# Performance work log

Measured on AMD Instinct MI355X. Metric: run time of the kernel, lower is better.

The kernel has to match this reference:

```python
import jax, jax.numpy as jnp
import numpy as np
import math

B, S, D, H = 8, 1024, 1024, 16
DH = D // H  # 64


def setup_inputs() -> dict:
    key = jax.random.key(0)
    ks = jax.random.split(key, 10)
    inputs = jax.random.normal(ks[0], (B, S, D), dtype=jnp.float32)
    mask = jax.random.randint(ks[1], (B, S, S), 0, 2) == 1  # bool [B,S,S]
    sc = 1.0 / math.sqrt(D)
    # per-head projection weights stacked: [H, D, DH], biases [H, DH]
    Wq = jax.random.normal(ks[2], (H, D, DH), dtype=jnp.float32) * sc
    bq = jax.random.normal(ks[3], (H, DH), dtype=jnp.float32) * 0.02
    Wk = jax.random.normal(ks[4], (H, D, DH), dtype=jnp.float32) * sc
    bk = jax.random.normal(ks[5], (H, DH), dtype=jnp.float32) * 0.02
    Wv = jax.random.normal(ks[6], (H, D, DH), dtype=jnp.float32) * sc
    bv = jax.random.normal(ks[7], (H, DH), dtype=jnp.float32) * 0.02
    Wo = jax.random.normal(ks[8], (D, D), dtype=jnp.float32) * sc
    bo = jax.random.normal(ks[9], (D,), dtype=jnp.float32) * 0.02
    return {"inputs": inputs, "mask": mask, "Wq": Wq, "bq": bq, "Wk": Wk,
            "bk": bk, "Wv": Wv, "bv": bv, "Wo": Wo, "bo": bo}


def reference(inputs, mask, Wq, bq, Wk, bk, Wv, bv, Wo, bo):
    d_model = inputs.shape[-1]
    scale = 1.0 / jnp.sqrt(jnp.asarray(d_model, inputs.dtype))  # note: sqrt(d_model), as in source
    # batched per-head projections: [B,H,S,DH]
    Q = jnp.einsum('bsd,hde->bhse', inputs, Wq) + bq[None, :, None, :]
    K = jnp.einsum('bsd,hde->bhse', inputs, Wk) + bk[None, :, None, :]
    V = jnp.einsum('bsd,hde->bhse', inputs, Wv) + bv[None, :, None, :]
    scores = jnp.einsum('bhse,bhte->bhst', Q, K) * scale  # [B,H,S,S]
    scores = jnp.where(mask[:, None, :, :], jnp.asarray(-1e9, scores.dtype), scores)
    attn = jax.nn.softmax(scores, axis=-1)
    ctx = jnp.einsum('bhst,bhte->bhse', attn, V)  # [B,H,S,DH]
    # concat heads along last dim (head h -> slice h*DH:(h+1)*DH), matches torch.cat
    bsz, h, s, dh = ctx.shape
    x = ctx.transpose(0, 2, 1, 3).reshape(bsz, s, h * dh)
    return x @ Wo + bo
```

## Files before the change

kernel.cpp:

```cpp
#include <hip/hip_runtime.h>
#include <hip/hip_bf16.h>
#include <stdint.h>


typedef __attribute__((ext_vector_type(8))) short short8;
typedef __attribute__((ext_vector_type(4))) float floatx4;

__device__ __forceinline__ int swz(int r, int kc) { return r * 8 + (kc ^ (r & 7)); }
__device__ __forceinline__ short8 as_frag(uint4 u) { return __builtin_bit_cast(short8, u); }
__device__ __forceinline__ floatx4 mfma16(short8 a, short8 b, floatx4 c) {
    return __builtin_amdgcn_mfma_f32_16x16x32_bf16(a, b, c, 0, 0, 0);
}
__device__ __forceinline__ unsigned short f2bu(float f) {
    return __builtin_bit_cast(unsigned short, __float2bfloat16(f));
}
__device__ __forceinline__ short f2b(float f) {
    return __builtin_bit_cast(short, __float2bfloat16(f));
}
__device__ __forceinline__ float b2f(short s) {
    return __bfloat162float(__builtin_bit_cast(__hip_bfloat16, s));
}
__device__ __forceinline__ void dma16(const void* g, void* l) {
    __builtin_amdgcn_global_load_lds(
        (const __attribute__((address_space(1))) uint32_t*)g,
        (__attribute__((address_space(3))) uint32_t*)l, 16, 0, 0);
}
__device__ __forceinline__ uint2 pack4(float a, float b, float c, float d) {
    uint2 p;
    p.x = (unsigned)f2bu(a) | ((unsigned)f2bu(b) << 16);
    p.y = (unsigned)f2bu(c) | ((unsigned)f2bu(d) << 16);
    return p;
}

__device__ __forceinline__ void detect_mode(const unsigned* Xw, int* s_is32) {
    if (threadIdx.x < 64) {
        unsigned lo = Xw[threadIdx.x] & 0xFFFFu;
        unsigned e = (lo >> 7) & 0xFFu;
        unsigned long long bal = __ballot(e >= 88u && e <= 150u);
        if (threadIdx.x == 0) *s_is32 = (bal != ~0ull) ? 1 : 0;
    }
    __syncthreads();
}

__device__ __forceinline__ float load_elt(const void* p, size_t idx, int is32) {
    return is32 ? ((const float*)p)[idx]
                : __bfloat162float(((const __hip_bfloat16*)p)[idx]);
}

__global__ __launch_bounds__(256) void transpose_weights(
    const void* __restrict__ Wq, const void* __restrict__ Wk,
    const void* __restrict__ Wv, const void* __restrict__ Wo,
    const unsigned* __restrict__ Xw,
    __hip_bfloat16* __restrict__ WT, __hip_bfloat16* __restrict__ WoT)
{
    __shared__ int s_is32;
    detect_mode(Xw, &s_is32);
    __shared__ __hip_bfloat16 T[64][72];
    int blk = blockIdx.x;
    const void* src; size_t src_off;
    __hip_bfloat16* dst;
    int src_ld, dst_ld;
    if (blk < 768) {
        int p = blk >> 8;
        int rem = blk & 255;
        int h = rem >> 4, dt = rem & 15;
        src = (p == 0) ? Wq : (p == 1) ? Wk : Wv;
        src_off = ((size_t)h * 1024 + (size_t)dt * 64) * 64;
        dst = WT + (((size_t)p * 16 + h) * 64) * 1024 + dt * 64;
        src_ld = 64; dst_ld = 1024;
    } else {
        int t = blk - 768;
        int kt = t >> 4, nt = t & 15;
        src = Wo; src_off = (size_t)kt * 64 * 1024 + nt * 64;
        dst = WoT + (size_t)nt * 64 * 1024 + kt * 64;
        src_ld = 1024; dst_ld = 1024;
    }
    int tid = threadIdx.x;
    #pragma unroll
    for (int i = 0; i < 16; i++) {
        int idx = tid + i * 256;
        int r = idx >> 6, c = idx & 63;
        T[c][r] = __float2bfloat16(load_elt(src, src_off + (size_t)r * src_ld + c, s_is32));
    }
    __syncthreads();
    #pragma unroll
    for (int i = 0; i < 16; i++) {
        int idx = tid + i * 256;
        int r = idx >> 6, c = idx & 63;
        dst[(size_t)r * dst_ld + c] = T[r][c];
    }
}

__global__ __launch_bounds__(256) void convert_bias(
    const void* __restrict__ bq, const void* __restrict__ bk,
    const void* __restrict__ bv, const void* __restrict__ bo,
    const unsigned* __restrict__ Xw, __hip_bfloat16* __restrict__ bc)
{
    __shared__ int s_is32;
    detect_mode(Xw, &s_is32);
    int tid = threadIdx.x;
    #pragma unroll
    for (int i = 0; i < 16; i++) {
        int idx = tid + i * 256;
        int which = idx >> 10, j = idx & 1023;
        const void* src = (which == 0) ? bq : (which == 1) ? bk : (which == 2) ? bv : bo;
        bc[idx] = __float2bfloat16(load_elt(src, j, s_is32));
    }
}

__global__ __launch_bounds__(256) void prep_mask(
    const void* __restrict__ mask_raw, unsigned long long* __restrict__ bits64)
{
    const int* mi = (const int*)mask_raw;
    const unsigned char* mb = (const unsigned char*)mask_raw;
    int tid = threadIdx.x, lane = tid & 63;
    bool ok = true;
    #pragma unroll
    for (int i = 0; i < 4; i++) {
        unsigned v = (unsigned)mi[lane * 4 + i];
        if (v > 1u) ok = false;
    }
    bool is_i32 = (__ballot(ok) == ~0ull);
    int gw = (blockIdx.x * 256 + tid) >> 6;
    const int NW = 512 * 4;
    const int NWORDS = (8 * 1024 * 1024) / 64;
    if (is_i32) {
        for (int i = gw; i < NWORDS; i += NW) {
            int mv = mi[(size_t)i * 64 + lane];
            unsigned long long bal = __ballot(mv != 0);
            if (lane == 0) bits64[i] = bal;
        }
    } else {
        for (int i = gw; i < NWORDS; i += NW) {
            int mv = mb[(size_t)i * 64 + lane];
            unsigned long long bal = __ballot(mv != 0);
            if (lane == 0) bits64[i] = bal;
        }
    }
}

__global__ __launch_bounds__(256) void convert_x(
    const void* __restrict__ X, __hip_bfloat16* __restrict__ Xb)
{
    __shared__ int s_is32;
    detect_mode((const unsigned*)X, &s_is32);
    size_t g = ((size_t)blockIdx.x * 256 + threadIdx.x) * 16;
    if (s_is32) {
        const float* Xf = (const float*)X;
        #pragma unroll
        for (int half = 0; half < 2; half++) {
            float4 f0 = *(const float4*)(Xf + g + half * 8);
            float4 f1 = *(const float4*)(Xf + g + half * 8 + 4);
            short8 s;
            s[0] = f2b(f0.x); s[1] = f2b(f0.y); s[2] = f2b(f0.z); s[3] = f2b(f0.w);
            s[4] = f2b(f1.x); s[5] = f2b(f1.y); s[6] = f2b(f1.z); s[7] = f2b(f1.w);
            *(uint4*)(Xb + g + half * 8) = __builtin_bit_cast(uint4, s);
        }
    } else {
        const uint4* Xu = (const uint4*)X;
        *(uint4*)(Xb + g)     = Xu[g / 8];
        *(uint4*)(Xb + g + 8) = Xu[g / 8 + 1];
    }
}

__global__ __launch_bounds__(256) void qkv_gemm_dma(
    const __hip_bfloat16* __restrict__ Xb,
    const __hip_bfloat16* __restrict__ WT,
    const __hip_bfloat16* __restrict__ bc,
    __hip_bfloat16* __restrict__ Q,
    __hip_bfloat16* __restrict__ Ko,
    __hip_bfloat16* __restrict__ Vt)
{
    __shared__ uint4 AsU[128 * 8];
    __shared__ uint4 BsU[128 * 8];
    int tid = threadIdx.x, lane = tid & 63, wave = tid >> 6;
    int quad = lane >> 4, ln = lane & 15;
    int m0 = blockIdx.x * 128;
    int n0 = blockIdx.y * 128;
    const __hip_bfloat16* Wp = WT + (size_t)n0 * 1024;

    floatx4 acc[2][8];
    #pragma unroll
    for (int i = 0; i < 2; i++)
        #pragma unroll
        for (int j = 0; j < 8; j++) acc[i][j] = (floatx4){0.f, 0.f, 0.f, 0.f};

    for (int k0 = 0; k0 < 1024; k0 += 64) {
        #pragma unroll
        for (int i = 0; i < 4; i++) {
            int r = wave * 32 + i * 8 + (lane >> 3);
            int kc = (lane & 7) ^ (r & 7);
            char* ldsA = (char*)AsU + (size_t)(wave * 256 + i * 64) * 16;
            char* ldsB = (char*)BsU + (size_t)(wave * 256 + i * 64) * 16;
            dma16(Xb + (size_t)(m0 + r) * 1024 + k0 + kc * 8, ldsA);
            dma16(Wp + (size_t)r * 1024 + k0 + kc * 8, ldsB);
        }
        __syncthreads();
        #pragma unroll
        for (int kk = 0; kk < 2; kk++) {
            short8 a0 = as_frag(AsU[swz(wave * 32 + ln, kk * 4 + quad)]);
            short8 a1 = as_frag(AsU[swz(wave * 32 + 16 + ln, kk * 4 + quad)]);
            #pragma unroll
            for (int nt = 0; nt < 8; nt++) {
                short8 bf = as_frag(BsU[swz(nt * 16 + ln, kk * 4 + quad)]);
                acc[0][nt] = mfma16(a0, bf, acc[0][nt]);
                acc[1][nt] = mfma16(a1, bf, acc[1][nt]);
            }
        }
        __syncthreads();
    }

    int b = m0 >> 10;
    int s0 = m0 & 1023;
    int proj = n0 >> 10;
    if (proj == 2) {
        #pragma unroll
        for (int nt = 0; nt < 8; nt++) {
            int n = n0 + nt * 16 + ln;
            int h = (n >> 6) & 15, e = n & 63;
            float bval = __bfloat162float(bc[2 * 1024 + (n & 1023)]);
            #pragma unroll
            for (int mt = 0; mt < 2; mt++) {
                int sb = s0 + wave * 32 + mt * 16 + quad * 4;
                uint2 pk = pack4(acc[mt][nt][0] + bval, acc[mt][nt][1] + bval,
                                 acc[mt][nt][2] + bval, acc[mt][nt][3] + bval);
                *(uint2*)(Vt + (((size_t)b * 16 + h) * 64 + e) * 1024 + sb) = pk;
            }
        }
    } else {
        __hip_bfloat16* P = (proj == 0) ? Q : Ko;
        #pragma unroll
        for (int nt = 0; nt < 8; nt++) {
            int n = n0 + nt * 16 + ln;
            int h = (n >> 6) & 15, e = n & 63;
            float bval = __bfloat162float(bc[proj * 1024 + (n & 1023)]);
            #pragma unroll
            for (int mt = 0; mt < 2; mt++) {
                #pragma unroll
                for (int r = 0; r < 4; r++) {
                    int s = s0 + wave * 32 + mt * 16 + quad * 4 + r;
                    P[(((size_t)b * 16 + h) * 1024 + s) * 64 + e] =
                        __float2bfloat16(acc[mt][nt][r] + bval);
                }
            }
        }
    }
}

__global__ __launch_bounds__(256) void qkv_gemm2(
    const void* __restrict__ Xsrc,
    const __hip_bfloat16* __restrict__ WT,
    const __hip_bfloat16* __restrict__ bc,
    __hip_bfloat16* __restrict__ Q,
    __hip_bfloat16* __restrict__ Ko,
    __hip_bfloat16* __restrict__ Vt)
{
    __shared__ int s_is32;
    detect_mode((const unsigned*)Xsrc, &s_is32);
    __shared__ uint4 AsU[128 * 8];
    __shared__ uint4 BsU[128 * 8];
    int tid = threadIdx.x, lane = tid & 63, wave = tid >> 6;
    int quad = lane >> 4, ln = lane & 15;
    int m0 = blockIdx.x * 128;
    int n0 = blockIdx.y * 128;
    const __hip_bfloat16* Wp = WT + (size_t)n0 * 1024;
    const float* Xf = (const float*)Xsrc;
    const __hip_bfloat16* Xh = (const __hip_bfloat16*)Xsrc;

    floatx4 acc[2][8];
    #pragma unroll
    for (int i = 0; i < 2; i++)
        #pragma unroll
        for (int j = 0; j < 8; j++) acc[i][j] = (floatx4){0.f, 0.f, 0.f, 0.f};

    for (int k0 = 0; k0 < 1024; k0 += 64) {
        if (s_is32) {
            #pragma unroll
            for (int i = 0; i < 4; i++) {
                int id = tid + i * 256;
                int r = id >> 3, kc = id & 7;
                size_t off = (size_t)(m0 + r) * 1024 + k0 + kc * 8;
                float4 f0 = *(const float4*)(Xf + off);
                float4 f1 = *(const float4*)(Xf + off + 4);
                short8 s;
                s[0] = f2b(f0.x); s[1] = f2b(f0.y); s[2] = f2b(f0.z); s[3] = f2b(f0.w);
                s[4] = f2b(f1.x); s[5] = f2b(f1.y); s[6] = f2b(f1.z); s[7] = f2b(f1.w);
                AsU[swz(r, kc)] = __builtin_bit_cast(uint4, s);
            }
        } else {
            #pragma unroll
            for (int i = 0; i < 4; i++) {
                int id = tid + i * 256;
                int r = id >> 3, kc = id & 7;
                AsU[swz(r, kc)] = *(const uint4*)(Xh + (size_t)(m0 + r) * 1024 + k0 + kc * 8);
            }
        }
        #pragma unroll
        for (int i = 0; i < 4; i++) {
            int id = tid + i * 256;
            int r = id >> 3, kc = id & 7;
            BsU[swz(r, kc)] = *(const uint4*)(Wp + (size_t)r * 1024 + k0 + kc * 8);
        }
        __syncthreads();
        #pragma unroll
        for (int kk = 0; kk < 2; kk++) {
            short8 a0 = as_frag(AsU[swz(wave * 32 + ln, kk * 4 + quad)]);
            short8 a1 = as_frag(AsU[swz(wave * 32 + 16 + ln, kk * 4 + quad)]);
            #pragma unroll
            for (int nt = 0; nt < 8; nt++) {
                short8 bf = as_frag(BsU[swz(nt * 16 + ln, kk * 4 + quad)]);
                acc[0][nt] = mfma16(a0, bf, acc[0][nt]);
                acc[1][nt] = mfma16(a1, bf, acc[1][nt]);
            }
        }
        __syncthreads();
    }

    int b = m0 >> 10;
    int s0 = m0 & 1023;
    #pragma unroll
    for (int nt = 0; nt < 8; nt++) {
        int n = n0 + nt * 16 + ln;
        int proj = n >> 10, h = (n >> 6) & 15, e = n & 63;
        float bval = __bfloat162float(bc[proj * 1024 + (n & 1023)]);
        #pragma unroll
        for (int mt = 0; mt < 2; mt++) {
            #pragma unroll
            for (int r = 0; r < 4; r++) {
                int s = s0 + wave * 32 + mt * 16 + quad * 4 + r;
                float v = acc[mt][nt][r] + bval;
                if (proj == 2) {
                    Vt[(((size_t)b * 16 + h) * 64 + e) * 1024 + s] = __float2bfloat16(v);
                } else {
                    __hip_bfloat16* P = (proj == 0) ? Q : Ko;
                    P[(((size_t)b * 16 + h) * 1024 + s) * 64 + e] = __float2bfloat16(v);
                }
            }
        }
    }
}

__global__ __launch_bounds__(256) void attn(
    const __hip_bfloat16* __restrict__ Q,
    const __hip_bfloat16* __restrict__ K,
    const __hip_bfloat16* __restrict__ Vt,
    const unsigned long long* __restrict__ bits,
    __hip_bfloat16* __restrict__ ctx)
{
    __shared__ uint4 QsU[128 * 8];
    __shared__ uint4 KsU[64 * 8];
    __shared__ uint4 VsU[64 * 8];
    __shared__ __hip_bfloat16 Ps[4 * 32 * 72];
    __shared__ unsigned long long Ms[128];

    int tid = threadIdx.x, lane = tid & 63, wave = tid >> 6;
    int quad = lane >> 4, ln = lane & 15;
    int bh = blockIdx.x;
    int q0 = blockIdx.y * 128;
    int b = bh >> 4, h = bh & 15;
    const __hip_bfloat16* Qp = Q + (size_t)bh * 1024 * 64;
    const __hip_bfloat16* Kp = K + (size_t)bh * 1024 * 64;
    const __hip_bfloat16* Vp = Vt + (size_t)bh * 64 * 1024;
    const unsigned long long* bp = bits + (size_t)b * 1024 * 16;

    #pragma unroll
    for (int i = 0; i < 4; i++) {
        int r = wave * 32 + i * 8 + (lane >> 3);
        int kc = (lane & 7) ^ (r & 7);
        char* lds = (char*)QsU + (size_t)(wave * 256 + i * 64) * 16;
        dma16(Qp + (size_t)(q0 + r) * 64 + kc * 8, lds);
    }
    __syncthreads();
    short8 qf[2][2];
    #pragma unroll
    for (int g = 0; g < 2; g++)
        #pragma unroll
        for (int kk = 0; kk < 2; kk++)
            qf[g][kk] = as_frag(QsU[swz(wave * 32 + g * 16 + ln, kk * 4 + quad)]);

    floatx4 acc_o[2][4];
    #pragma unroll
    for (int g = 0; g < 2; g++)
        #pragma unroll
        for (int i = 0; i < 4; i++) acc_o[g][i] = (floatx4){0.f, 0.f, 0.f, 0.f};
    float lsum[2] = {0.f, 0.f};
    const float scale = 0.03125f;
    __hip_bfloat16* Pw = Ps + wave * (32 * 72);

    for (int t0 = 0; t0 < 1024; t0 += 64) {
        __syncthreads();
        #pragma unroll
        for (int i = 0; i < 2; i++) {
            int r = (wave * 2 + i) * 8 + (lane >> 3);
            int kc = (lane & 7) ^ (r & 7);
            char* ldsK = (char*)KsU + (size_t)((wave * 2 + i) * 64) * 16;
            char* ldsV = (char*)VsU + (size_t)((wave * 2 + i) * 64) * 16;
            dma16(Kp + (size_t)(t0 + r) * 64 + kc * 8, ldsK);
            dma16(Vp + (size_t)r * 1024 + t0 + kc * 8, ldsV);
        }
        if (tid < 128)
            Ms[tid] = bp[(size_t)(q0 + tid) * 16 + (t0 >> 6)];
        __syncthreads();

        floatx4 st[2][4];
        #pragma unroll
        for (int g = 0; g < 2; g++)
            #pragma unroll
            for (int i = 0; i < 4; i++) st[g][i] = (floatx4){0.f, 0.f, 0.f, 0.f};
        #pragma unroll
        for (int kk = 0; kk < 2; kk++) {
            #pragma unroll
            for (int tt = 0; tt < 4; tt++) {
                short8 kf = as_frag(KsU[swz(tt * 16 + ln, kk * 4 + quad)]);
                st[0][tt] = mfma16(kf, qf[0][kk], st[0][tt]);
                st[1][tt] = mfma16(kf, qf[1][kk], st[1][tt]);
            }
        }

        #pragma unroll
        for (int g = 0; g < 2; g++) {
            unsigned long long mw = Ms[wave * 32 + g * 16 + ln];
            #pragma unroll
            for (int tt = 0; tt < 4; tt++) {
                unsigned mb = (unsigned)(mw >> (tt * 16 + quad * 4)) & 0xFu;
                float pe0 = (mb & 1u) ? 0.f : __expf(st[g][tt][0] * scale);
                float pe1 = (mb & 2u) ? 0.f : __expf(st[g][tt][1] * scale);
                float pe2 = (mb & 4u) ? 0.f : __expf(st[g][tt][2] * scale);
                float pe3 = (mb & 8u) ? 0.f : __expf(st[g][tt][3] * scale);
                lsum[g] += (pe0 + pe1) + (pe2 + pe3);
                *(uint2*)(Pw + (g * 16 + ln) * 72 + tt * 16 + quad * 4) =
                    pack4(pe0, pe1, pe2, pe3);
            }
        }

        #pragma unroll
        for (int kk = 0; kk < 2; kk++) {
            short8 pf0 = as_frag(*(const uint4*)(Pw + (0 * 16 + ln) * 72 + kk * 32 + quad * 8));
            short8 pf1 = as_frag(*(const uint4*)(Pw + (1 * 16 + ln) * 72 + kk * 32 + quad * 8));
            #pragma unroll
            for (int et = 0; et < 4; et++) {
                short8 vf = as_frag(VsU[swz(et * 16 + ln, kk * 4 + quad)]);
                acc_o[0][et] = mfma16(vf, pf0, acc_o[0][et]);
                acc_o[1][et] = mfma16(vf, pf1, acc_o[1][et]);
            }
        }
    }

    #pragma unroll
    for (int g = 0; g < 2; g++) {
        lsum[g] += __shfl_xor(lsum[g], 16, 64);
        lsum[g] += __shfl_xor(lsum[g], 32, 64);
    }
    float inv[2];
    inv[0] = 1.f / fmaxf(lsum[0], 1e-20f);
    inv[1] = 1.f / fmaxf(lsum[1], 1e-20f);

    #pragma unroll
    for (int g = 0; g < 2; g++) {
        int s = q0 + wave * 32 + g * 16 + ln;
        __hip_bfloat16* crow = ctx + ((size_t)b * 1024 + s) * 1024 + h * 64 + quad * 4;
        #pragma unroll
        for (int et = 0; et < 4; et++) {
            uint2 pk = pack4(acc_o[g][et][0] * inv[g], acc_o[g][et][1] * inv[g],
                             acc_o[g][et][2] * inv[g], acc_o[g][et][3] * inv[g]);
            *(uint2*)(crow + et * 16) = pk;
        }
    }
}

__global__ __launch_bounds__(256) void out_gemm_dma(
    const __hip_bfloat16* __restrict__ Cx,
    const __hip_bfloat16* __restrict__ WoT,
    const __hip_bfloat16* __restrict__ bc,
    const unsigned* __restrict__ Xw,
    void* __restrict__ dout,
    int direct)
{
    __shared__ int s_is32;
    detect_mode(Xw, &s_is32);
    __shared__ uint4 AsU[128 * 8];
    __shared__ uint4 BsU[128 * 8];
    int tid = threadIdx.x, lane = tid & 63, wave = tid >> 6;
    int quad = lane >> 4, ln = lane & 15;
    int m0 = blockIdx.x * 128;
    int n0 = blockIdx.y * 128;

    floatx4 acc[2][8];
    #pragma unroll
    for (int i = 0; i < 2; i++)
        #pragma unroll
        for (int j = 0; j < 8; j++) acc[i][j] = (floatx4){0.f, 0.f, 0.f, 0.f};

    for (int k0 = 0; k0 < 1024; k0 += 64) {
        #pragma unroll
        for (int i = 0; i < 4; i++) {
            int r = wave * 32 + i * 8 + (lane >> 3);
            int kc = (lane & 7) ^ (r & 7);
            char* ldsA = (char*)AsU + (size_t)(wave * 256 + i * 64) * 16;
            char* ldsB = (char*)BsU + (size_t)(wave * 256 + i * 64) * 16;
            dma16(Cx + (size_t)(m0 + r) * 1024 + k0 + kc * 8, ldsA);
            dma16(WoT + (size_t)(n0 + r) * 1024 + k0 + kc * 8, ldsB);
        }
        __syncthreads();
        #pragma unroll
        for (int kk = 0; kk < 2; kk++) {
            short8 a0 = as_frag(AsU[swz(wave * 32 + ln, kk * 4 + quad)]);
            short8 a1 = as_frag(AsU[swz(wave * 32 + 16 + ln, kk * 4 + quad)]);
            #pragma unroll
            for (int nt = 0; nt < 8; nt++) {
                short8 bf = as_frag(BsU[swz(nt * 16 + ln, kk * 4 + quad)]);
                acc[0][nt] = mfma16(a0, bf, acc[0][nt]);
                acc[1][nt] = mfma16(a1, bf, acc[1][nt]);
            }
        }
        __syncthreads();
    }

    const __hip_bfloat16* bo = bc + 3 * 1024;
    #pragma unroll
    for (int nt = 0; nt < 8; nt++) {
        int n = n0 + nt * 16 + ln;
        float bval = __bfloat162float(bo[n]);
        #pragma unroll
        for (int mt = 0; mt < 2; mt++) {
            #pragma unroll
            for (int r = 0; r < 4; r++) {
                int m = m0 + wave * 32 + mt * 16 + quad * 4 + r;
                float v = acc[mt][nt][r] + bval;
                if (direct && s_is32) ((float*)dout)[(size_t)m * 1024 + n] = v;
                else ((__hip_bfloat16*)dout)[(size_t)m * 1024 + n] = __float2bfloat16(v);
            }
        }
    }
}

__global__ __launch_bounds__(256) void emit_out(
    const __hip_bfloat16* __restrict__ Fo, const unsigned* __restrict__ Xw,
    void* __restrict__ dout)
{
    __shared__ int s_is32;
    detect_mode(Xw, &s_is32);
    size_t g = (size_t)blockIdx.x * 256 + threadIdx.x;
    uint4 u = *(const uint4*)(Fo + g * 8);
    if (s_is32) {
        short8 s = __builtin_bit_cast(short8, u);
        float4 f0, f1;
        f0.x = b2f(s[0]); f0.y = b2f(s[1]); f0.z = b2f(s[2]); f0.w = b2f(s[3]);
        f1.x = b2f(s[4]); f1.y = b2f(s[5]); f1.z = b2f(s[6]); f1.w = b2f(s[7]);
        *(float4*)((float*)dout + g * 8) = f0;
        *(float4*)((float*)dout + g * 8 + 4) = f1;
    } else {
        *(uint4*)((__hip_bfloat16*)dout + g * 8) = u;
    }
}

extern "C" void kernel_launch(void* const* d_in, const int* in_sizes, int n_in,
                              void* d_out, int out_size, void* d_ws, size_t ws_size,
                              hipStream_t stream) {
    const void* X  = d_in[0];
    const void* mk = d_in[1];
    const void* Wq = d_in[2];
    const void* bq = d_in[3];
    const void* Wk = d_in[4];
    const void* bk = d_in[5];
    const void* Wv = d_in[6];
    const void* bv = d_in[7];
    const void* Wo = d_in[8];
    const void* bo = d_in[9];
    const unsigned* Xw = (const unsigned*)X;

    char* ws = (char*)d_ws;
    __hip_bfloat16*     WT   = (__hip_bfloat16*)(ws);
    __hip_bfloat16*     WoT  = (__hip_bfloat16*)(ws + ((size_t)6 << 20));
    unsigned long long* bits = (unsigned long long*)(ws + ((size_t)8 << 20));
    __hip_bfloat16*     bc   = (__hip_bfloat16*)(ws + ((size_t)9 << 20));
    __hip_bfloat16*     Xb   = (__hip_bfloat16*)(ws + ((size_t)10 << 20));
    __hip_bfloat16*     Qb   = (__hip_bfloat16*)(ws + ((size_t)26 << 20));
    __hip_bfloat16*     Kb   = (__hip_bfloat16*)(ws + ((size_t)42 << 20));
    __hip_bfloat16*     Vtb  = (__hip_bfloat16*)(ws + ((size_t)58 << 20));

    bool bigws = ws_size >= ((size_t)74 << 20);

    hipLaunchKernelGGL(transpose_weights, dim3(1024), dim3(256), 0, stream,
                       Wq, Wk, Wv, Wo, Xw, WT, WoT);
    hipLaunchKernelGGL(convert_bias, dim3(1), dim3(256), 0, stream,
                       bq, bk, bv, bo, Xw, bc);
    hipLaunchKernelGGL(prep_mask, dim3(512), dim3(256), 0, stream, mk, bits);

    if (bigws) {
        __hip_bfloat16* Cx = Xb;
        hipLaunchKernelGGL(convert_x, dim3(2048), dim3(256), 0, stream, X, Xb);
        hipLaunchKernelGGL(qkv_gemm_dma, dim3(64, 24), dim3(256), 0, stream,
                           Xb, WT, bc, Qb, Kb, Vtb);
        hipLaunchKernelGGL(attn, dim3(128, 8), dim3(256), 0, stream,
                           Qb, Kb, Vtb, bits, Cx);
        hipLaunchKernelGGL(out_gemm_dma, dim3(64, 8), dim3(256), 0, stream,
                           Cx, WoT, bc, Xw, d_out, 1);
    } else {
        __hip_bfloat16* Cx = (__hip_bfloat16*)d_out;
        __hip_bfloat16* Fo = Qb;
        hipLaunchKernelGGL(qkv_gemm2, dim3(64, 24), dim3(256), 0, stream,
                           X, WT, bc, Qb, Kb, Vtb);
        hipLaunchKernelGGL(attn, dim3(128, 8), dim3(256), 0, stream,
                           Qb, Kb, Vtb, bits, Cx);
        hipLaunchKernelGGL(out_gemm_dma, dim3(64, 8), dim3(256), 0, stream,
                           Cx, WoT, bc, Xw, (void*)Fo, 0);
        hipLaunchKernelGGL(emit_out, dim3(4096), dim3(256), 0, stream,
                           Fo, Xw, d_out);
    }
}
```

Measured before the change: 334.8 us.

## Fuse prep kernels and retile QKV, attention, and output GEMMs

Merges the weight transpose, bias conversion, mask bit-packing and X conversion into one launch, which removes three launches. The QKV GEMM now uses 256x128 block tiles with a 2x2 wave grid, so each wave holds 8x4 accumulators and reuses its A and B fragments more. The attention kernel runs two waves of 64 query rows each, with a swizzled P buffer in shared memory. The output GEMM uses a 2x2 wave layout. The cost is higher register pressure and fewer blocks in the QKV and attention kernels, which can lower occupancy.

```diff
diff --git a/kernel.cpp b/kernel.cpp
--- a/kernel.cpp
+++ b/kernel.cpp
@@ -47,123 +47,116 @@
                 : __bfloat162float(((const __hip_bfloat16*)p)[idx]);
 }
 
-__global__ __launch_bounds__(256) void transpose_weights(
+__global__ __launch_bounds__(256) void prep_all(
     const void* __restrict__ Wq, const void* __restrict__ Wk,
     const void* __restrict__ Wv, const void* __restrict__ Wo,
-    const unsigned* __restrict__ Xw,
-    __hip_bfloat16* __restrict__ WT, __hip_bfloat16* __restrict__ WoT)
-{
-    __shared__ int s_is32;
-    detect_mode(Xw, &s_is32);
-    __shared__ __hip_bfloat16 T[64][72];
-    int blk = blockIdx.x;
-    const void* src; size_t src_off;
-    __hip_bfloat16* dst;
-    int src_ld, dst_ld;
-    if (blk < 768) {
-        int p = blk >> 8;
-        int rem = blk & 255;
-        int h = rem >> 4, dt = rem & 15;
-        src = (p == 0) ? Wq : (p == 1) ? Wk : Wv;
-        src_off = ((size_t)h * 1024 + (size_t)dt * 64) * 64;
-        dst = WT + (((size_t)p * 16 + h) * 64) * 1024 + dt * 64;
-        src_ld = 64; dst_ld = 1024;
-    } else {
-        int t = blk - 768;
-        int kt = t >> 4, nt = t & 15;
-        src = Wo; src_off = (size_t)kt * 64 * 1024 + nt * 64;
-        dst = WoT + (size_t)nt * 64 * 1024 + kt * 64;
-        src_ld = 1024; dst_ld = 1024;
-    }
-    int tid = threadIdx.x;
-    #pragma unroll
-    for (int i = 0; i < 16; i++) {
-        int idx = tid + i * 256;
-        int r = idx >> 6, c = idx & 63;
-        T[c][r] = __float2bfloat16(load_elt(src, src_off + (size_t)r * src_ld + c, s_is32));
-    }
-    __syncthreads();
-    #pragma unroll
-    for (int i = 0; i < 16; i++) {
-        int idx = tid + i * 256;
-        int r = idx >> 6, c = idx & 63;
-        dst[(size_t)r * dst_ld + c] = T[r][c];
-    }
-}
-
-__global__ __launch_bounds__(256) void convert_bias(
     const void* __restrict__ bq, const void* __restrict__ bk,
     const void* __restrict__ bv, const void* __restrict__ bo,
-    const unsigned* __restrict__ Xw, __hip_bfloat16* __restrict__ bc)
+    const void* __restrict__ mask_raw, const void* __restrict__ X,
+    __hip_bfloat16* __restrict__ WT, __hip_bfloat16* __restrict__ WoT,
+    __hip_bfloat16* __restrict__ bc, unsigned long long* __restrict__ bits64,
+    __hip_bfloat16* __restrict__ Xb, int do_x)
 {
+    __shared__ __hip_bfloat16 T[64][72];
     __shared__ int s_is32;
-    detect_mode(Xw, &s_is32);
+    int blk = blockIdx.x;
     int tid = threadIdx.x;
-    #pragma unroll
-    for (int i = 0; i < 16; i++) {
-        int idx = tid + i * 256;
-        int which = idx >> 10, j = idx & 1023;
-        const void* src = (which == 0) ? bq : (which == 1) ? bk : (which == 2) ? bv : bo;
-        bc[idx] = __float2bfloat16(load_elt(src, j, s_is32));
-    }
-}
-
-__global__ __launch_bounds__(256) void prep_mask(
-    const void* __restrict__ mask_raw, unsigned long long* __restrict__ bits64)
-{
-    const int* mi = (const int*)mask_raw;
-    const unsigned char* mb = (const unsigned char*)mask_raw;
-    int tid = threadIdx.x, lane = tid & 63;
-    bool ok = true;
-    #pragma unroll
-    for (int i = 0; i < 4; i++) {
-        unsigned v = (unsigned)mi[lane * 4 + i];
-        if (v > 1u) ok = false;
-    }
-    bool is_i32 = (__ballot(ok) == ~0ull);
-    int gw = (blockIdx.x * 256 + tid) >> 6;
-    const int NW = 512 * 4;
-    const int NWORDS = (8 * 1024 * 1024) / 64;
-    if (is_i32) {
-        for (int i = gw; i < NWORDS; i += NW) {
-            int mv = mi[(size_t)i * 64 + lane];
-            unsigned long long bal = __ballot(mv != 0);
-            if (lane == 0) bits64[i] = bal;
-        }
-    } else {
-        for (int i = gw; i < NWORDS; i += NW) {
-            int mv = mb[(size_t)i * 64 + lane];
-            unsigned long long bal = __ballot(mv != 0);
-            if (lane == 0) bits64[i] = bal;
-        }
-    }
-}
-
-__global__ __launch_bounds__(256) void convert_x(
-    const void* __restrict__ X, __hip_bfloat16* __restrict__ Xb)
-{
-    __shared__ int s_is32;
-    detect_mode((const unsigned*)X, &s_is32);
-    size_t g = ((size_t)blockIdx.x * 256 + threadIdx.x) * 16;
-    if (s_is32) {
-        const float* Xf = (const float*)X;
-        #pragma unroll
-        for (int half = 0; half < 2; half++) {
-            float4 f0 = *(const float4*)(Xf + g + half * 8);
-            float4 f1 = *(const float4*)(Xf + g + half * 8 + 4);
-            short8 s;
-            s[0] = f2b(f0.x); s[1] = f2b(f0.y); s[2] = f2b(f0.z); s[3] = f2b(f0.w);
-            s[4] = f2b(f1.x); s[5] = f2b(f1.y); s[6] = f2b(f1.z); s[7] = f2b(f1.w);
-            *(uint4*)(Xb + g + half * 8) = __builtin_bit_cast(uint4, s);
-        }
-    } else {
-        const uint4* Xu = (const uint4*)X;
-        *(uint4*)(Xb + g)     = Xu[g / 8];
-        *(uint4*)(Xb + g + 8) = Xu[g / 8 + 1];
-    }
-}
-
-__global__ __launch_bounds__(256) void qkv_gemm_dma(
+    const unsigned* Xw = (const unsigned*)X;
+
+    if (blk < 1024) {
+        detect_mode(Xw, &s_is32);
+        const void* src; size_t src_off;
+        __hip_bfloat16* dst;
+        int src_ld, dst_ld;
+        if (blk < 768) {
+            int p = blk >> 8;
+            int rem = blk & 255;
+            int h = rem >> 4, dt = rem & 15;
+            src = (p == 0) ? Wq : (p == 1) ? Wk : Wv;
+            src_off = ((size_t)h * 1024 + (size_t)dt * 64) * 64;
+            dst = WT + (((size_t)p * 16 + h) * 64) * 1024 + dt * 64;
+            src_ld = 64; dst_ld = 1024;
+        } else {
+            int t = blk - 768;
+            int kt = t >> 4, nt = t & 15;
+            src = Wo; src_off = (size_t)kt * 64 * 1024 + nt * 64;
+            dst = WoT + (size_t)nt * 64 * 1024 + kt * 64;
+            src_ld = 1024; dst_ld = 1024;
+        }
+        #pragma unroll
+        for (int i = 0; i < 16; i++) {
+            int idx = tid + i * 256;
+            int r = idx >> 6, c = idx & 63;
+            T[c][r] = __float2bfloat16(load_elt(src, src_off + (size_t)r * src_ld + c, s_is32));
+        }
+        __syncthreads();
+        #pragma unroll
+        for (int i = 0; i < 16; i++) {
+            int idx = tid + i * 256;
+            int r = idx >> 6, c = idx & 63;
+            dst[(size_t)r * dst_ld + c] = T[r][c];
+        }
+    } else if (blk == 1024) {
+        detect_mode(Xw, &s_is32);
+        #pragma unroll
+        for (int i = 0; i < 16; i++) {
+            int idx = tid + i * 256;
+            int which = idx >> 10, j = idx & 1023;
+            const void* src = (which == 0) ? bq : (which == 1) ? bk : (which == 2) ? bv : bo;
+            bc[idx] = __float2bfloat16(load_elt(src, j, s_is32));
+        }
+    } else if (blk < 1537) {
+        int blkL = blk - 1025;
+        const int* mi = (const int*)mask_raw;
+        const unsigned char* mb = (const unsigned char*)mask_raw;
+        int lane = tid & 63;
+        bool ok = true;
+        #pragma unroll
+        for (int i = 0; i < 4; i++) {
+            unsigned v = (unsigned)mi[lane * 4 + i];
+            if (v > 1u) ok = false;
+        }
+        bool is_i32 = (__ballot(ok) == ~0ull);
+        int gw = (blkL * 256 + tid) >> 6;
+        const int NW = 512 * 4;
+        const int NWORDS = (8 * 1024 * 1024) / 64;
+        if (is_i32) {
+            for (int i = gw; i < NWORDS; i += NW) {
+                int mv = mi[(size_t)i * 64 + lane];
+                unsigned long long bal = __ballot(mv != 0);
+                if (lane == 0) bits64[i] = bal;
+            }
+        } else {
+            for (int i = gw; i < NWORDS; i += NW) {
+                int mv = mb[(size_t)i * 64 + lane];
+                unsigned long long bal = __ballot(mv != 0);
+                if (lane == 0) bits64[i] = bal;
+            }
+        }
+    } else if (do_x) {
+        detect_mode(Xw, &s_is32);
+        int blkL = blk - 1537;
+        size_t g = ((size_t)blkL * 256 + tid) * 16;
+        if (s_is32) {
+            const float* Xf = (const float*)X;
+            #pragma unroll
+            for (int half = 0; half < 2; half++) {
+                float4 f0 = *(const float4*)(Xf + g + half * 8);
+                float4 f1 = *(const float4*)(Xf + g + half * 8 + 4);
+                short8 s;
+                s[0] = f2b(f0.x); s[1] = f2b(f0.y); s[2] = f2b(f0.z); s[3] = f2b(f0.w);
+                s[4] = f2b(f1.x); s[5] = f2b(f1.y); s[6] = f2b(f1.z); s[7] = f2b(f1.w);
+                *(uint4*)(Xb + g + half * 8) = __builtin_bit_cast(uint4, s);
+            }
+        } else {
+            const uint4* Xu = (const uint4*)X;
+            *(uint4*)(Xb + g)     = Xu[g / 8];
+            *(uint4*)(Xb + g + 8) = Xu[g / 8 + 1];
+        }
+    }
+}
+
+__global__ __launch_bounds__(256, 2) void qkv_gemm_dma(
     const __hip_bfloat16* __restrict__ Xb,
     const __hip_bfloat16* __restrict__ WT,
     const __hip_bfloat16* __restrict__ bc,
@@ -171,41 +164,51 @@
     __hip_bfloat16* __restrict__ Ko,
     __hip_bfloat16* __restrict__ Vt)
 {
-    __shared__ uint4 AsU[128 * 8];
+    __shared__ uint4 AsU[256 * 8];
     __shared__ uint4 BsU[128 * 8];
     int tid = threadIdx.x, lane = tid & 63, wave = tid >> 6;
     int quad = lane >> 4, ln = lane & 15;
-    int m0 = blockIdx.x * 128;
+    int mw = wave & 1, nw = wave >> 1;
+    int m0 = blockIdx.x * 256;
     int n0 = blockIdx.y * 128;
     const __hip_bfloat16* Wp = WT + (size_t)n0 * 1024;
 
-    floatx4 acc[2][8];
-    #pragma unroll
-    for (int i = 0; i < 2; i++)
-        #pragma unroll
-        for (int j = 0; j < 8; j++) acc[i][j] = (floatx4){0.f, 0.f, 0.f, 0.f};
+    floatx4 acc[8][4];
+    #pragma unroll
+    for (int i = 0; i < 8; i++)
+        #pragma unroll
+        for (int j = 0; j < 4; j++) acc[i][j] = (floatx4){0.f, 0.f, 0.f, 0.f};
 
     for (int k0 = 0; k0 < 1024; k0 += 64) {
+        #pragma unroll
+        for (int i = 0; i < 8; i++) {
+            int r = wave * 64 + i * 8 + (lane >> 3);
+            int kc = (lane & 7) ^ (r & 7);
+            char* lds = (char*)AsU + (size_t)(wave * 512 + i * 64) * 16;
+            dma16(Xb + (size_t)(m0 + r) * 1024 + k0 + kc * 8, lds);
+        }
         #pragma unroll
         for (int i = 0; i < 4; i++) {
             int r = wave * 32 + i * 8 + (lane >> 3);
             int kc = (lane & 7) ^ (r & 7);
-            char* ldsA = (char*)AsU + (size_t)(wave * 256 + i * 64) * 16;
-            char* ldsB = (char*)BsU + (size_t)(wave * 256 + i * 64) * 16;
-            dma16(Xb + (size_t)(m0 + r) * 1024 + k0 + kc * 8, ldsA);
-            dma16(Wp + (size_t)r * 1024 + k0 + kc * 8, ldsB);
+            char* lds = (char*)BsU + (size_t)(wave * 256 + i * 64) * 16;
+            dma16(Wp + (size_t)r * 1024 + k0 + kc * 8, lds);
         }
         __syncthreads();
         #pragma unroll
         for (int kk = 0; kk < 2; kk++) {
-            short8 a0 = as_frag(AsU[swz(wave * 32 + ln, kk * 4 + quad)]);
-            short8 a1 = as_frag(AsU[swz(wave * 32 + 16 + ln, kk * 4 + quad)]);
-            #pragma unroll
-            for (int nt = 0; nt < 8; nt++) {
-                short8 bf = as_frag(BsU[swz(nt * 16 + ln, kk * 4 + quad)]);
-                acc[0][nt] = mfma16(a0, bf, acc[0][nt]);
-                acc[1][nt] = mfma16(a1, bf, acc[1][nt]);
-            }
+            short8 af[8], bf[4];
+            #pragma unroll
+            for (int mi = 0; mi < 8; mi++)
+                af[mi] = as_frag(AsU[swz(mw * 128 + mi * 16 + ln, kk * 4 + quad)]);
+            #pragma unroll
+            for (int ni = 0; ni < 4; ni++)
+                bf[ni] = as_frag(BsU[swz(nw * 64 + ni * 16 + ln, kk * 4 + quad)]);
+            #pragma unroll
+            for (int mi = 0; mi < 8; mi++)
+                #pragma unroll
+                for (int ni = 0; ni < 4; ni++)
+                    acc[mi][ni] = mfma16(af[mi], bf[ni], acc[mi][ni]);
         }
         __syncthreads();
     }
@@ -215,32 +218,32 @@
     int proj = n0 >> 10;
     if (proj == 2) {
         #pragma unroll
-        for (int nt = 0; nt < 8; nt++) {
-            int n = n0 + nt * 16 + ln;
+        for (int ni = 0; ni < 4; ni++) {
+            int n = n0 + nw * 64 + ni * 16 + ln;
             int h = (n >> 6) & 15, e = n & 63;
             float bval = __bfloat162float(bc[2 * 1024 + (n & 1023)]);
             #pragma unroll
-            for (int mt = 0; mt < 2; mt++) {
-                int sb = s0 + wave * 32 + mt * 16 + quad * 4;
-                uint2 pk = pack4(acc[mt][nt][0] + bval, acc[mt][nt][1] + bval,
-                                 acc[mt][nt][2] + bval, acc[mt][nt][3] + bval);
+            for (int mi = 0; mi < 8; mi++) {
+                int sb = s0 + mw * 128 + mi * 16 + quad * 4;
+                uint2 pk = pack4(acc[mi][ni][0] + bval, acc[mi][ni][1] + bval,
+                                 acc[mi][ni][2] + bval, acc[mi][ni][3] + bval);
                 *(uint2*)(Vt + (((size_t)b * 16 + h) * 64 + e) * 1024 + sb) = pk;
             }
         }
     } else {
         __hip_bfloat16* P = (proj == 0) ? Q : Ko;
         #pragma unroll
-        for (int nt = 0; nt < 8; nt++) {
-            int n = n0 + nt * 16 + ln;
+        for (int ni = 0; ni < 4; ni++) {
+            int n = n0 + nw * 64 + ni * 16 + ln;
             int h = (n >> 6) & 15, e = n & 63;
             float bval = __bfloat162float(bc[proj * 1024 + (n & 1023)]);
             #pragma unroll
-            for (int mt = 0; mt < 2; mt++) {
+            for (int mi = 0; mi < 8; mi++) {
                 #pragma unroll
                 for (int r = 0; r < 4; r++) {
-                    int s = s0 + wave * 32 + mt * 16 + quad * 4 + r;
+                    int s = s0 + mw * 128 + mi * 16 + quad * 4 + r;
                     P[(((size_t)b * 16 + h) * 1024 + s) * 64 + e] =
-                        __float2bfloat16(acc[mt][nt][r] + bval);
+                        __float2bfloat16(acc[mi][ni][r] + bval);
                 }
             }
         }
@@ -340,7 +343,7 @@
     }
 }
 
-__global__ __launch_bounds__(256) void attn(
+__global__ __launch_bounds__(128) void attn(
     const __hip_bfloat16* __restrict__ Q,
     const __hip_bfloat16* __restrict__ K,
     const __hip_bfloat16* __restrict__ Vt,
@@ -350,10 +353,10 @@
     __shared__ uint4 QsU[128 * 8];
     __shared__ uint4 KsU[64 * 8];
     __shared__ uint4 VsU[64 * 8];
-    __shared__ __hip_bfloat16 Ps[4 * 32 * 72];
+    __shared__ uint4 PsU[2 * 64 * 8];
     __shared__ unsigned long long Ms[128];
 
-    int tid = threadIdx.x, lane = tid & 63, wave = tid >> 6;
+    int tid = threadIdx.x, lane = tid & 63, w = tid >> 6;
     int quad = lane >> 4, ln = lane & 15;
     int bh = blockIdx.x;
     int q0 = blockIdx.y * 128;
@@ -364,47 +367,46 @@
     const unsigned long long* bp = bits + (size_t)b * 1024 * 16;
 
     #pragma unroll
-    for (int i = 0; i < 4; i++) {
-        int r = wave * 32 + i * 8 + (lane >> 3);
+    for (int i = 0; i < 8; i++) {
+        int r = w * 64 + i * 8 + (lane >> 3);
         int kc = (lane & 7) ^ (r & 7);
-        char* lds = (char*)QsU + (size_t)(wave * 256 + i * 64) * 16;
+        char* lds = (char*)QsU + (size_t)(w * 512 + i * 64) * 16;
         dma16(Qp + (size_t)(q0 + r) * 64 + kc * 8, lds);
     }
     __syncthreads();
-    short8 qf[2][2];
-    #pragma unroll
-    for (int g = 0; g < 2; g++)
+    short8 qf[4][2];
+    #pragma unroll
+    for (int g = 0; g < 4; g++)
         #pragma unroll
         for (int kk = 0; kk < 2; kk++)
-            qf[g][kk] = as_frag(QsU[swz(wave * 32 + g * 16 + ln, kk * 4 + quad)]);
-
-    floatx4 acc_o[2][4];
-    #pragma unroll
-    for (int g = 0; g < 2; g++)
+            qf[g][kk] = as_frag(QsU[swz(w * 64 + g * 16 + ln, kk * 4 + quad)]);
+
+    floatx4 acc_o[4][4];
+    #pragma unroll
+    for (int g = 0; g < 4; g++)
         #pragma unroll
         for (int i = 0; i < 4; i++) acc_o[g][i] = (floatx4){0.f, 0.f, 0.f, 0.f};
-    float lsum[2] = {0.f, 0.f};
+    float lsum[4] = {0.f, 0.f, 0.f, 0.f};
     const float scale = 0.03125f;
-    __hip_bfloat16* Pw = Ps + wave * (32 * 72);
+    __hip_bfloat16* Pw = (__hip_bfloat16*)&PsU[w * 512];
 
     for (int t0 = 0; t0 < 1024; t0 += 64) {
         __syncthreads();
         #pragma unroll
-        for (int i = 0; i < 2; i++) {
-            int r = (wave * 2 + i) * 8 + (lane >> 3);
+        for (int i = 0; i < 4; i++) {
+            int r = w * 32 + i * 8 + (lane >> 3);
             int kc = (lane & 7) ^ (r & 7);
-            char* ldsK = (char*)KsU + (size_t)((wave * 2 + i) * 64) * 16;
-            char* ldsV = (char*)VsU + (size_t)((wave * 2 + i) * 64) * 16;
+            char* ldsK = (char*)KsU + (size_t)(w * 256 + i * 64) * 16;
+            char* ldsV = (char*)VsU + (size_t)(w * 256 + i * 64) * 16;
             dma16(Kp + (size_t)(t0 + r) * 64 + kc * 8, ldsK);
             dma16(Vp + (size_t)r * 1024 + t0 + kc * 8, ldsV);
         }
-        if (tid < 128)
-            Ms[tid] = bp[(size_t)(q0 + tid) * 16 + (t0 >> 6)];
-        __syncthreads();
-
-        floatx4 st[2][4];
-        #pragma unroll
-        for (int g = 0; g < 2; g++)
+        Ms[tid] = bp[(size_t)(q0 + tid) * 16 + (t0 >> 6)];
+        __syncthreads();
+
+        floatx4 st[4][4];
+        #pragma unroll
+        for (int g = 0; g < 4; g++)
             #pragma unroll
             for (int i = 0; i < 4; i++) st[g][i] = (floatx4){0.f, 0.f, 0.f, 0.f};
         #pragma unroll
@@ -412,14 +414,16 @@
             #pragma unroll
             for (int tt = 0; tt < 4; tt++) {
                 short8 kf = as_frag(KsU[swz(tt * 16 + ln, kk * 4 + quad)]);
-                st[0][tt] = mfma16(kf, qf[0][kk], st[0][tt]);
-                st[1][tt] = mfma16(kf, qf[1][kk], st[1][tt]);
-            }
-        }
-
-        #pragma unroll
-        for (int g = 0; g < 2; g++) {
-            unsigned long long mw = Ms[wave * 32 + g * 16 + ln];
+                #pragma unroll
+                for (int g = 0; g < 4; g++)
+                    st[g][tt] = mfma16(kf, qf[g][kk], st[g][tt]);
+            }
+        }
+
+        #pragma unroll
+        for (int g = 0; g < 4; g++) {
+            int qloc = g * 16 + ln;
+            unsigned long long mw = Ms[w * 64 + qloc];
             #pragma unroll
             for (int tt = 0; tt < 4; tt++) {
                 unsigned mb = (unsigned)(mw >> (tt * 16 + quad * 4)) & 0xFu;
@@ -428,41 +432,43 @@
                 float pe2 = (mb & 4u) ? 0.f : __expf(st[g][tt][2] * scale);
                 float pe3 = (mb & 8u) ? 0.f : __expf(st[g][tt][3] * scale);
                 lsum[g] += (pe0 + pe1) + (pe2 + pe3);
-                *(uint2*)(Pw + (g * 16 + ln) * 72 + tt * 16 + quad * 4) =
-                    pack4(pe0, pe1, pe2, pe3);
+                int kc = tt * 2 + (quad >> 1);
+                int off = qloc * 64 + (kc ^ (qloc & 7)) * 8 + (quad & 1) * 4;
+                *(uint2*)(Pw + off) = pack4(pe0, pe1, pe2, pe3);
             }
         }
 
         #pragma unroll
         for (int kk = 0; kk < 2; kk++) {
-            short8 pf0 = as_frag(*(const uint4*)(Pw + (0 * 16 + ln) * 72 + kk * 32 + quad * 8));
-            short8 pf1 = as_frag(*(const uint4*)(Pw + (1 * 16 + ln) * 72 + kk * 32 + quad * 8));
+            short8 pf[4];
+            #pragma unroll
+            for (int g = 0; g < 4; g++)
+                pf[g] = as_frag(PsU[w * 512 + swz(g * 16 + ln, kk * 4 + quad)]);
             #pragma unroll
             for (int et = 0; et < 4; et++) {
                 short8 vf = as_frag(VsU[swz(et * 16 + ln, kk * 4 + quad)]);
-                acc_o[0][et] = mfma16(vf, pf0, acc_o[0][et]);
-                acc_o[1][et] = mfma16(vf, pf1, acc_o[1][et]);
-            }
-        }
-    }
-
-    #pragma unroll
-    for (int g = 0; g < 2; g++) {
+                #pragma unroll
+                for (int g = 0; g < 4; g++)
+                    acc_o[g][et] = mfma16(vf, pf[g], acc_o[g][et]);
+            }
+        }
+    }
+
+    #pragma unroll
+    for (int g = 0; g < 4; g++) {
         lsum[g] += __shfl_xor(lsum[g], 16, 64);
         lsum[g] += __shfl_xor(lsum[g], 32, 64);
     }
-    float inv[2];
-    inv[0] = 1.f / fmaxf(lsum[0], 1e-20f);
-    inv[1] = 1.f / fmaxf(lsum[1], 1e-20f);
-
-    #pragma unroll
-    for (int g = 0; g < 2; g++) {
-        int s = q0 + wave * 32 + g * 16 + ln;
+
+    #pragma unroll
+    for (int g = 0; g < 4; g++) {
+        float inv = 1.f / fmaxf(lsum[g], 1e-20f);
+        int s = q0 + w * 64 + g * 16 + ln;
         __hip_bfloat16* crow = ctx + ((size_t)b * 1024 + s) * 1024 + h * 64 + quad * 4;
         #pragma unroll
         for (int et = 0; et < 4; et++) {
-            uint2 pk = pack4(acc_o[g][et][0] * inv[g], acc_o[g][et][1] * inv[g],
-                             acc_o[g][et][2] * inv[g], acc_o[g][et][3] * inv[g]);
+            uint2 pk = pack4(acc_o[g][et][0] * inv, acc_o[g][et][1] * inv,
+                             acc_o[g][et][2] * inv, acc_o[g][et][3] * inv);
             *(uint2*)(crow + et * 16) = pk;
         }
     }
@@ -482,14 +488,15 @@
     __shared__ uint4 BsU[128 * 8];
     int tid = threadIdx.x, lane = tid & 63, wave = tid >> 6;
     int quad = lane >> 4, ln = lane & 15;
+    int mw = wave & 1, nw = wave >> 1;
     int m0 = blockIdx.x * 128;
     int n0 = blockIdx.y * 128;
 
-    floatx4 acc[2][8];
-    #pragma unroll
-    for (int i = 0; i < 2; i++)
-        #pragma unroll
-        for (int j = 0; j < 8; j++) acc[i][j] = (floatx4){0.f, 0.f, 0.f, 0.f};
+    floatx4 acc[4][4];
+    #pragma unroll
+    for (int i = 0; i < 4; i++)
+        #pragma unroll
+        for (int j = 0; j < 4; j++) acc[i][j] = (floatx4){0.f, 0.f, 0.f, 0.f};
 
     for (int k0 = 0; k0 < 1024; k0 += 64) {
         #pragma unroll
@@ -504,29 +511,33 @@
         __syncthreads();
         #pragma unroll
         for (int kk = 0; kk < 2; kk++) {
-            short8 a0 = as_frag(AsU[swz(wave * 32 + ln, kk * 4 + quad)]);
-            short8 a1 = as_frag(AsU[swz(wave * 32 + 16 + ln, kk * 4 + quad)]);
-            #pragma unroll
-            for (int nt = 0; nt < 8; nt++) {
-                short8 bf = as_frag(BsU[swz(nt * 16 + ln, kk * 4 + quad)]);
-                acc[0][nt] = mfma16(a0, bf, acc[0][nt]);
-                acc[1][nt] = mfma16(a1, bf, acc[1][nt]);
-            }
+            short8 af[4], bf[4];
+            #pragma unroll
+            for (int mi = 0; mi < 4; mi++)
+                af[mi] = as_frag(AsU[swz(mw * 64 + mi * 16 + ln, kk * 4 + quad)]);
+            #pragma unroll
+            for (int ni = 0; ni < 4; ni++)
+                bf[ni] = as_frag(BsU[swz(nw * 64 + ni * 16 + ln, kk * 4 + quad)]);
+            #pragma unroll
+            for (int mi = 0; mi < 4; mi++)
+                #pragma unroll
+                for (int ni = 0; ni < 4; ni++)
+                    acc[mi][ni] = mfma16(af[mi], bf[ni], acc[mi][ni]);
         }
         __syncthreads();
     }
 
     const __hip_bfloat16* bo = bc + 3 * 1024;
     #pragma unroll
-    for (int nt = 0; nt < 8; nt++) {
-        int n = n0 + nt * 16 + ln;
+    for (int ni = 0; ni < 4; ni++) {
+        int n = n0 + nw * 64 + ni * 16 + ln;
         float bval = __bfloat162float(bo[n]);
         #pragma unroll
-        for (int mt = 0; mt < 2; mt++) {
+        for (int mi = 0; mi < 4; mi++) {
             #pragma unroll
             for (int r = 0; r < 4; r++) {
-                int m = m0 + wave * 32 + mt * 16 + quad * 4 + r;
-                float v = acc[mt][nt][r] + bval;
+                int m = m0 + mw * 64 + mi * 16 + quad * 4 + r;
+                float v = acc[mi][ni][r] + bval;
                 if (direct && s_is32) ((float*)dout)[(size_t)m * 1024 + n] = v;
                 else ((__hip_bfloat16*)dout)[(size_t)m * 1024 + n] = __float2bfloat16(v);
             }
@@ -581,18 +592,15 @@
 
     bool bigws = ws_size >= ((size_t)74 << 20);
 
-    hipLaunchKernelGGL(transpose_weights, dim3(1024), dim3(256), 0, stream,
-                       Wq, Wk, Wv, Wo, Xw, WT, WoT);
-    hipLaunchKernelGGL(convert_bias, dim3(1), dim3(256), 0, stream,
-                       bq, bk, bv, bo, Xw, bc);
-    hipLaunchKernelGGL(prep_mask, dim3(512), dim3(256), 0, stream, mk, bits);
+    hipLaunchKernelGGL(prep_all, dim3(3585), dim3(256), 0, stream,
+                       Wq, Wk, Wv, Wo, bq, bk, bv, bo, mk, X,
+                       WT, WoT, bc, bits, Xb, bigws ? 1 : 0);
 
     if (bigws) {
         __hip_bfloat16* Cx = Xb;
-        hipLaunchKernelGGL(convert_x, dim3(2048), dim3(256), 0, stream, X, Xb);
-        hipLaunchKernelGGL(qkv_gemm_dma, dim3(64, 24), dim3(256), 0, stream,
+        hipLaunchKernelGGL(qkv_gemm_dma, dim3(32, 24), dim3(256), 0, stream,
                            Xb, WT, bc, Qb, Kb, Vtb);
-        hipLaunchKernelGGL(attn, dim3(128, 8), dim3(256), 0, stream,
+        hipLaunchKernelGGL(attn, dim3(128, 8), dim3(128), 0, stream,
                            Qb, Kb, Vtb, bits, Cx);
         hipLaunchKernelGGL(out_gemm_dma, dim3(64, 8), dim3(256), 0, stream,
                            Cx, WoT, bc, Xw, d_out, 1);
@@ -601,7 +609,7 @@
         __hip_bfloat16* Fo = Qb;
         hipLaunchKernelGGL(qkv_gemm2, dim3(64, 24), dim3(256), 0, stream,
                            X, WT, bc, Qb, Kb, Vtb);
-        hipLaunchKernelGGL(attn, dim3(128, 8), dim3(256), 0, stream,
+        hipLaunchKernelGGL(attn, dim3(128, 8), dim3(128), 0, stream,
                            Qb, Kb, Vtb, bits, Cx);
         hipLaunchKernelGGL(out_gemm_dma, dim3(64, 8), dim3(256), 0, stream,
                            Cx, WoT, bc, Xw, (void*)Fo, 0);
```

Measured after the change: 343.8 us. 2.7% more time.
